# Performance work log

Hardware: AMD Instinct MI355X
Metric: run time of the kernel (lower is better)

The kernel has to match this reference:

```python
import jax, jax.numpy as jnp
import numpy as np
from jax import lax

B, CIN, COUT, H, W = 2, 256, 128, 128, 128
PPI = 4  # pixels_per_iter


def setup_inputs() -> dict:
    key = jax.random.key(0)
    ks = jax.random.split(key, 10)
    p = lambda k, shp: jax.random.normal(k, shp, jnp.float32) * 0.05
    return {
        "x": jax.random.normal(ks[0], (B, CIN, H, W), jnp.float32),
        "grads": jax.random.normal(ks[1], (B, 2, H, W), jnp.float32),
        "w1": p(ks[2], (COUT, CIN, 1, 1)),          # conv1x1 (bias=False, resnet-style)
        "w2": p(ks[3], (COUT, CIN, 1, 1)),
        "merge_dw": p(ks[4], (2 * COUT, 1, 3, 3)),   # depthwise 3x3
        "merge_pw": p(ks[5], (COUT, 2 * COUT, 1, 1)),# pointwise 1x1
        "merge_b": p(ks[6], (COUT,)),
        "post_dw": p(ks[7], (COUT, 1, 3, 3)),
        "post_pw": p(ks[8], (COUT, COUT, 1, 1)),
        "post_b": p(ks[9], (COUT,)),
    }


def conv2d(x, w, pad=0, groups=1):
    return lax.conv_general_dilated(x, w, (1, 1), [(pad, pad), (pad, pad)],
                                    feature_group_count=groups)


def base_grid(Bn, Hn, Wn):
    # torch affine_grid with identity theta, align_corners=True
    xs = jnp.linspace(-1.0, 1.0, Wn)
    ys = jnp.linspace(-1.0, 1.0, Hn)
    gx, gy = jnp.meshgrid(xs, ys)                      # [H,W] each
    g = jnp.stack([gx, gy], axis=-1)                   # [H,W,2], last dim = (x,y)
    return jnp.broadcast_to(g, (Bn, Hn, Wn, 2))


def grid_sample(img, grid):
    # bilinear, align_corners=True, padding_mode='zeros' (torch defaults)
    Bn, C, Hn, Wn = img.shape
    x = (grid[..., 0] + 1.0) * (Wn - 1) * 0.5          # [B,H,W] pixel coords
    y = (grid[..., 1] + 1.0) * (Hn - 1) * 0.5
    x0 = jnp.floor(x); y0 = jnp.floor(y)
    x1 = x0 + 1.0;     y1 = y0 + 1.0
    wx1 = x - x0; wx0 = 1.0 - wx1
    wy1 = y - y0; wy0 = 1.0 - wy1

    def corner(xi, yi, w):
        valid = (xi >= 0) & (xi <= Wn - 1) & (yi >= 0) & (yi <= Hn - 1)
        xc = jnp.clip(xi, 0, Wn - 1).astype(jnp.int32)
        yc = jnp.clip(yi, 0, Hn - 1).astype(jnp.int32)
        v = jax.vmap(lambda im, yy, xx: im[:, yy, xx])(img, yc, xc)  # [B,C,H,W]
        return v * (w * valid)[:, None]

    return (corner(x0, y0, wx0 * wy0) + corner(x1, y0, wx1 * wy0) +
            corner(x0, y1, wx0 * wy1) + corner(x1, y1, wx1 * wy1))


def reference(x, grads, w1, w2, merge_dw, merge_pw, merge_b, post_dw, post_pw, post_b):
    Bn, _, Hn, Wn = x.shape
    iters = 3 * Hn // (4 * PPI)
    g = (1.5 * grads / iters).transpose(0, 2, 3, 1)    # [B,H,W,2]
    grid = base_grid(Bn, Hn, Wn)
    grid1 = grid + g
    grid2 = grid - g

    m1 = jax.nn.sigmoid(conv2d(x, w1))
    m2 = jax.nn.sigmoid(conv2d(x, w2))

    def step(carry, _):
        a, b, sa, sb = carry
        a = grid_sample(a, grid1)
        b = grid_sample(b, grid2)
        return (a, b, sa + a, sb + b), None

    (_, _, s1, s2), _ = lax.scan(jax.checkpoint(step), (m1, m2, m1, m2), None, length=iters)

    m = jnp.concatenate([jax.nn.sigmoid(s1), jax.nn.sigmoid(s2)], axis=1)  # [B,2*COUT,H,W]
    m = conv2d(conv2d(m, merge_dw, pad=1, groups=2 * COUT), merge_pw) + merge_b[None, :, None, None]
    m = conv2d(conv2d(m, post_dw, pad=1, groups=COUT), post_pw) + post_b[None, :, None, None]
    return m
```

## Files before the change

### kernel.cpp

```cpp
#include <hip/hip_runtime.h>
#include <hip/hip_fp16.h>


#define PC 4194304
#define HW 16384

struct CoefC { int4 o0; float4 w0; int4 o1; float4 w1; int4 o2; float4 w2; int4 o3; float4 w3; };
struct Coef1 { int4 oa; float4 wa; };

struct alignas(16) H8 { __half2 h[4]; };
struct alignas(8)  H4 { __half2 h[2]; };
typedef _Float16 f16x8 __attribute__((ext_vector_type(8)));
typedef float f32x4 __attribute__((ext_vector_type(4)));

__device__ __forceinline__ float sigf(float v) { return 1.0f / (1.0f + __expf(-v)); }

__device__ __forceinline__ H8 f8h(const float* f) {
  H8 r;
#pragma unroll
  for (int i = 0; i < 4; i++) r.h[i] = __floats2half2_rn(f[2*i], f[2*i+1]);
  return r;
}
__device__ __forceinline__ f16x8 ld8(const __half* p) { return *(const f16x8*)p; }
__device__ __forceinline__ void fma8(float* a, const f16x8& v, float w) {
#pragma unroll
  for (int i = 0; i < 8; i++) a[i] = fmaf(w, (float)v[i], a[i]);
}
__device__ __forceinline__ void fma4g(float* a, const f16x8& v0, const f16x8& v1,
                                      const f16x8& v2, const f16x8& v3, float4 w) {
  fma8(a, v0, w.x); fma8(a, v1, w.y); fma8(a, v2, w.z); fma8(a, v3, w.w);
}

template <int SPB>
__device__ __forceinline__ int slot_base_64k(int bid) {
  int xcd = bid & 7;
  int i = xcd >> 1;
  int half = xcd & 1;
  int sub = bid >> 3;
  return (i >> 1) * 32768 + (i & 1) * 16384 + half * 8192 + sub * SPB;
}
template <int SPB>
__device__ __forceinline__ int slot_base_32k(int bid) {
  int xcd = bid & 7;
  int b = xcd >> 2;
  int q = xcd & 3;
  int sub = bid >> 3;
  return b * 16384 + q * 4096 + sub * SPB;
}

__device__ __forceinline__ void stencil(const float* __restrict__ g, float sgn, int pix,
                                        int4& op, float4& wt) {
  int b = pix >> 14, hw = pix & 16383;
  int h = hw >> 7, w = hw & 127;
  float gx = g[(size_t)(b * 2 + 0) * HW + hw];
  float gy = g[(size_t)(b * 2 + 1) * HW + hw];
  float xp = (float)w + sgn * gx;
  float yp = (float)h + sgn * gy;
  float x0f = floorf(xp), y0f = floorf(yp);
  float fx = xp - x0f, fy = yp - y0f;
  int x0 = (int)x0f, y0 = (int)y0f;
  int x1 = x0 + 1, y1 = y0 + 1;
  bool vx0 = (x0 >= 0) && (x0 <= 127);
  bool vx1 = (x1 >= 0) && (x1 <= 127);
  bool vy0 = (y0 >= 0) && (y0 <= 127);
  bool vy1 = (y1 >= 0) && (y1 <= 127);
  int x0c = min(max(x0, 0), 127), x1c = min(max(x1, 0), 127);
  int y0c = min(max(y0, 0), 127), y1c = min(max(y1, 0), 127);
  int bb = b << 14;
  op.x = bb + y0c * 128 + x0c;
  op.y = bb + y0c * 128 + x1c;
  op.z = bb + y1c * 128 + x0c;
  op.w = bb + y1c * 128 + x1c;
  wt.x = (vx0 && vy0) ? (1.f - fx) * (1.f - fy) : 0.f;
  wt.y = (vx1 && vy0) ? fx * (1.f - fy) : 0.f;
  wt.z = (vx0 && vy1) ? (1.f - fx) * fy : 0.f;
  wt.w = (vx1 && vy1) ? fx * fy : 0.f;
}

__device__ __forceinline__ int4 shl7(int4 v) {
  return make_int4(v.x << 7, v.y << 7, v.z << 7, v.w << 7);
}
__device__ __forceinline__ float4 scale4(float4 v, float s) {
  return make_float4(v.x * s, v.y * s, v.z * s, v.w * s);
}

__global__ __launch_bounds__(256) void prep_kernel(const float* __restrict__ grads,
                                                   Coef1* __restrict__ c1,
                                                   CoefC* __restrict__ c2,
                                                   const float* __restrict__ mdw,
                                                   const float* __restrict__ pdw,
                                                   const float* __restrict__ w1,
                                                   const float* __restrict__ w2,
                                                   const float* __restrict__ mpw,
                                                   const float* __restrict__ ppw,
                                                   float* __restrict__ wdwT,
                                                   float* __restrict__ pdwT,
                                                   __half* __restrict__ wT16,
                                                   __half* __restrict__ wpw1,
                                                   __half* __restrict__ wpw2) {
  int bid = blockIdx.x;
  int tid = threadIdx.x;
  if (bid < 256) {
    int idx = bid * 256 + tid;
    int chain = idx >> 15;
    int p = idx & 32767;
    float sgn = chain ? -3.96875f : 3.96875f;
    int4 op; float4 ow;
    stencil(grads, sgn, p, op, ow);
    Coef1 a; a.oa = shl7(op); a.wa = ow;
    c1[idx] = a;
    CoefC c;
    int4 o2; float4 nw;
    stencil(grads, sgn, op.x, o2, nw); c.o0 = shl7(o2); c.w0 = scale4(nw, ow.x);
    stencil(grads, sgn, op.y, o2, nw); c.o1 = shl7(o2); c.w1 = scale4(nw, ow.y);
    stencil(grads, sgn, op.z, o2, nw); c.o2 = shl7(o2); c.w2 = scale4(nw, ow.z);
    stencil(grads, sgn, op.w, o2, nw); c.o3 = shl7(o2); c.w3 = scale4(nw, ow.w);
    c2[idx] = c;
  } else {
    int i = (bid - 256) * 256 + tid;
    if (i < 65536) {
      int co = i >> 8, ci = i & 255;
      float v = (co < 128) ? w1[co * 256 + ci] : w2[(size_t)(co - 128) * 256 + ci];
      wT16[i] = __float2half(v);
    } else if (i < 98304) {
      int j = i - 65536;
      wpw1[j] = __float2half(mpw[j]);
    } else if (i < 114688) {
      int j = i - 98304;
      wpw2[j] = __float2half(ppw[j]);
    } else if (i < 116992) {
      int j = i - 114688;
      int ch = j / 9, t = j % 9;
      wdwT[t * 256 + ch] = mdw[j];
    } else if (i < 118144) {
      int j = i - 116992;
      int ch = j / 9, t = j % 9;
      pdwT[t * 128 + ch] = pdw[j];
    }
  }
}

__global__ __launch_bounds__(256) void conv1_kernel(const float* __restrict__ x,
                                                    const __half* __restrict__ wT16,
                                                    __half* __restrict__ mOut) {
  __shared__ __align__(16) char As[4096];
  __shared__ __align__(16) char Bs[16384];
  int tid = threadIdx.x;
  int p0 = blockIdx.x * 64;
  int b = p0 >> 14;
  int hw0 = p0 & 16383;
  int wv = tid >> 6, ln = tid & 63;
  int hi = ln >> 4, lo = ln & 15;
  f32x4 acc[4][4] = {};
  const float* xb = x + (size_t)b * 256 * HW + hw0;
  int apx = tid & 63, ac8 = (tid >> 6) * 8;
  int abyte = (apx * 64 + ac8 * 2) ^ ((apx & 3) << 4);
  for (int k = 0; k < 256; k += 32) {
    f16x8 av;
#pragma unroll
    for (int j = 0; j < 8; j++) av[j] = (_Float16)xb[(size_t)(k + ac8 + j) * HW + apx];
    if (k) __syncthreads();
    *(f16x8*)(As + abyte) = av;
    {
      const __half* src = wT16 + (size_t)tid * 256 + k;
#pragma unroll
      for (int s = 0; s < 4; s++) {
        f16x8 bv = *(const f16x8*)(src + s * 8);
        int byte = (tid * 64 + s * 16) ^ ((tid & 3) << 4);
        *(f16x8*)(Bs + byte) = bv;
      }
    }
    __syncthreads();
    f16x8 aF[4], bF[4];
#pragma unroll
    for (int m = 0; m < 4; m++) {
      int px = m * 16 + lo;
      int byte = (px * 64 + hi * 16) ^ ((px & 3) << 4);
      aF[m] = *(const f16x8*)(As + byte);
    }
#pragma unroll
    for (int n = 0; n < 4; n++) {
      int co = wv * 64 + n * 16 + lo;
      int byte = (co * 64 + hi * 16) ^ ((co & 3) << 4);
      bF[n] = *(const f16x8*)(Bs + byte);
    }
#pragma unroll
    for (int m = 0; m < 4; m++)
#pragma unroll
      for (int n = 0; n < 4; n++)
        acc[m][n] = __builtin_amdgcn_mfma_f32_16x16x32_f16(aF[m], bF[n], acc[m][n], 0, 0, 0);
  }
  size_t base = (wv >= 2) ? (size_t)PC : 0;
  int col0 = (wv & 1) * 64;
#pragma unroll
  for (int m = 0; m < 4; m++)
#pragma unroll
    for (int n = 0; n < 4; n++) {
      int col = col0 + n * 16 + lo;
#pragma unroll
      for (int rr = 0; rr < 4; rr++) {
        int px = p0 + m * 16 + hi * 4 + rr;
        mOut[base + (size_t)px * 128 + col] = __float2half(sigf(acc[m][n][rr]));
      }
    }
}

template <int ACC>
__global__ __launch_bounds__(256) void s2_kernel(const __half* __restrict__ inb,
                                                 __half* __restrict__ outb,
                                                 const __half* __restrict__ accAdd,
                                                 __half* __restrict__ accOut,
                                                 const uint4* __restrict__ c2tab) {
  __shared__ uint4 cs[128];
  int tid = threadIdx.x;
  int slot0 = slot_base_64k<16>(blockIdx.x);
  if (tid < 128) cs[tid] = c2tab[(size_t)slot0 * 8 + tid];
  __syncthreads();
  const CoefC c = ((const CoefC*)cs)[tid >> 4];
  int slot = slot0 + (tid >> 4);
  int ch = (tid & 15) << 3;
  int chain = slot >> 15;
  size_t cb = (size_t)chain * PC;
  const __half* base = inb + cb + ch;
  int rowel = ((slot & 32767) << 7) + ch;

  float a2[8] = {};
  f16x8 p0 = ld8(base + c.o0.x), p1 = ld8(base + c.o0.y),
        p2 = ld8(base + c.o0.z), p3 = ld8(base + c.o0.w);
  f16x8 q0 = ld8(base + c.o1.x), q1 = ld8(base + c.o1.y),
        q2 = ld8(base + c.o1.z), q3 = ld8(base + c.o1.w);
  fma4g(a2, p0, p1, p2, p3, c.w0);
  p0 = ld8(base + c.o2.x); p1 = ld8(base + c.o2.y);
  p2 = ld8(base + c.o2.z); p3 = ld8(base + c.o2.w);
  fma4g(a2, q0, q1, q2, q3, c.w1);
  q0 = ld8(base + c.o3.x); q1 = ld8(base + c.o3.y);
  q2 = ld8(base + c.o3.z); q3 = ld8(base + c.o3.w);
  fma4g(a2, p0, p1, p2, p3, c.w2);
  fma4g(a2, q0, q1, q2, q3, c.w3);

  if (ACC != 3) *(H8*)(outb + cb + rowel) = f8h(a2);
  if (ACC == 1 || ACC == 3) {
    f16x8 av = ld8(accAdd + cb + rowel);
    float af[8];
#pragma unroll
    for (int i = 0; i < 8; i++) af[i] = a2[i] + (float)av[i];
    *(H8*)(accOut + cb + rowel) = f8h(af);
  } else if (ACC == 2) {
    f16x8 av = ld8(accOut + cb + rowel);
    float af[8];
#pragma unroll
    for (int i = 0; i < 8; i++) af[i] = a2[i] + (float)av[i];
    *(H8*)(accOut + cb + rowel) = f8h(af);
  }
}

template <int MODE>
__global__ __launch_bounds__(256) void s1_kernel(const __half* __restrict__ tin,
                                                 const __half* __restrict__ own,
                                                 __half* __restrict__ outb,
                                                 const uint4* __restrict__ c1tab) {
  __shared__ uint4 cs[32];
  int tid = threadIdx.x;
  int slot0 = slot_base_64k<16>(blockIdx.x);
  if (tid < 32) cs[tid] = c1tab[(size_t)slot0 * 2 + tid];
  __syncthreads();
  const Coef1 a = ((const Coef1*)cs)[tid >> 4];
  int slot = slot0 + (tid >> 4);
  int ch = (tid & 15) << 3;
  int chain = slot >> 15;
  size_t cb = (size_t)chain * PC;
  const __half* base = tin + cb + ch;
  int rowel = ((slot & 32767) << 7) + ch;
  f16x8 t0 = ld8(base + a.oa.x), t1 = ld8(base + a.oa.y),
        t2 = ld8(base + a.oa.z), t3 = ld8(base + a.oa.w);
  f16x8 ov = ld8(own + cb + rowel);
  float r[8] = {};
  fma4g(r, t0, t1, t2, t3, a.wa);
  if (MODE == 0) {
#pragma unroll
    for (int i = 0; i < 8; i++) r[i] += (float)ov[i];
  } else {
#pragma unroll
    for (int i = 0; i < 8; i++) r[i] = sigf(r[i] + (float)ov[i]);
  }
  *(H8*)(outb + cb + rowel) = f8h(r);
}

template <int C>
__global__ __launch_bounds__(256) void dw_kernel(const __half* __restrict__ in,
                                                 const float* __restrict__ wT,
                                                 __half* __restrict__ out) {
  int tid = threadIdx.x;
  constexpr int TPP = C / 8;
  constexpr int PPB = 256 / TPP;
  int slot = slot_base_32k<PPB>(blockIdx.x) + tid / TPP;
  int ch = (tid % TPP) * 8;
  int b = slot >> 14, h = (slot >> 7) & 127, w = slot & 127;
  const __half* src;
  int choff;
  if (C == 256) { src = in + ((ch < 128) ? 0 : (size_t)PC); choff = ch & 127; }
  else          { src = in; choff = ch; }
  float acc[8] = {};
#pragma unroll
  for (int t = 0; t < 9; t++) {
    int dy = t / 3 - 1, dx = t % 3 - 1;
    int yy = h + dy, xx = w + dx;
    if (yy < 0 || yy > 127 || xx < 0 || xx > 127) continue;
    int q = (b << 14) + yy * 128 + xx;
    f16x8 v = ld8(src + (size_t)q * 128 + choff);
    float4 wa = *(const float4*)(wT + t * C + ch);
    float4 wb = *(const float4*)(wT + t * C + ch + 4);
    acc[0] = fmaf(wa.x, (float)v[0], acc[0]);
    acc[1] = fmaf(wa.y, (float)v[1], acc[1]);
    acc[2] = fmaf(wa.z, (float)v[2], acc[2]);
    acc[3] = fmaf(wa.w, (float)v[3], acc[3]);
    acc[4] = fmaf(wb.x, (float)v[4], acc[4]);
    acc[5] = fmaf(wb.y, (float)v[5], acc[5]);
    acc[6] = fmaf(wb.z, (float)v[6], acc[6]);
    acc[7] = fmaf(wb.w, (float)v[7], acc[7]);
  }
  *(H8*)(out + (size_t)slot * C + ch) = f8h(acc);
}

__global__ __launch_bounds__(256) void pw1_kernel(const __half* __restrict__ in,
                                                  const __half* __restrict__ w16,
                                                  const float* __restrict__ bias,
                                                  __half* __restrict__ out) {
  int tid = threadIdx.x;
  int p0 = blockIdx.x * 64;
  int wv = tid >> 6, ln = tid & 63;
  int hi = ln >> 4, lo = ln & 15;
  int px = p0 + wv * 16 + lo;
  f32x4 acc[8] = {};
  for (int k = 0; k < 256; k += 32) {
    f16x8 bF = *(const f16x8*)(in + (size_t)px * 256 + k + hi * 8);
#pragma unroll
    for (int m = 0; m < 8; m++) {
      f16x8 aF = *(const f16x8*)(w16 + (size_t)(m * 16 + lo) * 256 + k + hi * 8);
      acc[m] = __builtin_amdgcn_mfma_f32_16x16x32_f16(aF, bF, acc[m], 0, 0, 0);
    }
  }
  int opx = p0 + wv * 16 + lo;
#pragma unroll
  for (int m = 0; m < 8; m++) {
    int co = m * 16 + hi * 4;
    float4 bv = *(const float4*)(bias + co);
    H4 hv;
    hv.h[0] = __floats2half2_rn(acc[m][0] + bv.x, acc[m][1] + bv.y);
    hv.h[1] = __floats2half2_rn(acc[m][2] + bv.z, acc[m][3] + bv.w);
    *(H4*)(out + (size_t)opx * 128 + co) = hv;
  }
}

__global__ __launch_bounds__(256) void pw2_kernel(const __half* __restrict__ in,
                                                  const __half* __restrict__ w16,
                                                  const float* __restrict__ bias,
                                                  float* __restrict__ out) {
  int tid = threadIdx.x;
  int p0 = blockIdx.x * 64;
  int b = p0 >> 14;
  int hw0 = p0 & 16383;
  int wv = tid >> 6, ln = tid & 63;
  int hi = ln >> 4, lo = ln & 15;
  int co0 = wv * 32;
  f32x4 acc[4][2] = {};
  for (int k = 0; k < 128; k += 32) {
    f16x8 aF[4], bF[2];
#pragma unroll
    for (int m = 0; m < 4; m++)
      aF[m] = *(const f16x8*)(in + (size_t)(p0 + m * 16 + lo) * 128 + k + hi * 8);
#pragma unroll
    for (int n = 0; n < 2; n++)
      bF[n] = *(const f16x8*)(w16 + (size_t)(co0 + n * 16 + lo) * 128 + k + hi * 8);
#pragma unroll
    for (int m = 0; m < 4; m++)
#pragma unroll
      for (int n = 0; n < 2; n++)
        acc[m][n] = __builtin_amdgcn_mfma_f32_16x16x32_f16(aF[m], bF[n], acc[m][n], 0, 0, 0);
  }
#pragma unroll
  for (int m = 0; m < 4; m++)
#pragma unroll
    for (int n = 0; n < 2; n++) {
      int co = co0 + n * 16 + lo;
      float bb = bias[co];
      float4 v = {acc[m][n][0] + bb, acc[m][n][1] + bb, acc[m][n][2] + bb, acc[m][n][3] + bb};
      *(float4*)(out + (size_t)(b * 128 + co) * HW + hw0 + m * 16 + hi * 4) = v;
    }
}

extern "C" void kernel_launch(void* const* d_in, const int* in_sizes, int n_in,
                              void* d_out, int out_size, void* d_ws, size_t ws_size,
                              hipStream_t stream) {
  const float* x     = (const float*)d_in[0];
  const float* grads = (const float*)d_in[1];
  const float* w1    = (const float*)d_in[2];
  const float* w2    = (const float*)d_in[3];
  const float* mdw   = (const float*)d_in[4];
  const float* mpw   = (const float*)d_in[5];
  const float* mb    = (const float*)d_in[6];
  const float* pdw   = (const float*)d_in[7];
  const float* ppw   = (const float*)d_in[8];
  const float* pb    = (const float*)d_in[9];
  float* out = (float*)d_out;
  char* wsb = (char*)d_ws;

  __half* M  = (__half*)wsb;
  __half* A  = (__half*)(wsb + (size_t)16777216);
  __half* Bb = (__half*)(wsb + (size_t)33554432);
  __half* Pb = (__half*)(wsb + (size_t)50331648);
  __half* Qb = (__half*)(wsb + (size_t)67108864);
  CoefC* C2  = (CoefC*)(wsb + (size_t)83886080);
  Coef1* C1  = (Coef1*)(wsb + (size_t)92274688);
  __half* WT16 = (__half*)(wsb + (size_t)94371840);
  __half* WPW1 = (__half*)(wsb + (size_t)94502912);
  __half* WPW2 = (__half*)(wsb + (size_t)94568448);
  float* wdwT  = (float*)(wsb + (size_t)94601216);
  float* pdwT  = wdwT + 2304;

  const uint4* c2u = (const uint4*)C2;
  const uint4* c1u = (const uint4*)C1;

  prep_kernel<<<718, 256, 0, stream>>>(grads, C1, C2, mdw, pdw, w1, w2, mpw, ppw,
                                       wdwT, pdwT, WT16, WPW1, WPW2);
  conv1_kernel<<<512, 256, 0, stream>>>(x, WT16, M);

  s2_kernel<0><<<4096, 256, 0, stream>>>(M,  A,  nullptr, nullptr, c2u);
  s2_kernel<0><<<4096, 256, 0, stream>>>(A,  Bb, nullptr, nullptr, c2u);
  s2_kernel<0><<<4096, 256, 0, stream>>>(Bb, A,  nullptr, nullptr, c2u);
  s2_kernel<1><<<4096, 256, 0, stream>>>(A,  Bb, M,       Pb,      c2u);
  s2_kernel<0><<<4096, 256, 0, stream>>>(Bb, A,  nullptr, nullptr, c2u);
  s2_kernel<0><<<4096, 256, 0, stream>>>(A,  Bb, nullptr, nullptr, c2u);
  s2_kernel<0><<<4096, 256, 0, stream>>>(Bb, A,  nullptr, nullptr, c2u);
  s2_kernel<2><<<4096, 256, 0, stream>>>(A,  Bb, nullptr, Pb,      c2u);
  s2_kernel<0><<<4096, 256, 0, stream>>>(Pb, A,  nullptr, nullptr, c2u);
  s2_kernel<1><<<4096, 256, 0, stream>>>(A,  Bb, Pb,      Qb,      c2u);
  s2_kernel<3><<<4096, 256, 0, stream>>>(Qb, A,  Qb,      Pb,      c2u);
  s1_kernel<0><<<4096, 256, 0, stream>>>(Pb, Pb, Bb, c1u);
  s1_kernel<1><<<4096, 256, 0, stream>>>(Bb, M,  A,  c1u);

  __half* DW1 = Bb;
  __half* PW1 = Qb;
  __half* DW2 = Qb + PC;
  dw_kernel<256><<<4096, 256, 0, stream>>>(A, wdwT, DW1);
  pw1_kernel<<<512, 256, 0, stream>>>(DW1, WPW1, mb, PW1);
  dw_kernel<128><<<2048, 256, 0, stream>>>(PW1, pdwT, DW2);
  pw2_kernel<<<512, 256, 0, stream>>>(DW2, WPW2, pb, out);
}
```

Baseline: 269.0 us.

## Fuse depthwise 3x3 convs into pointwise MFMA kernels via swizzled LDS tiles

Merges each depthwise 3x3 conv with the following pointwise 1x1 MFMA GEMM into a single kernel. Each block computes an 8x8 pixel tile's depthwise outputs for all channels into XOR-swizzled shared memory, then runs the MFMA GEMM from LDS. This removes the global write and read of the DW1/DW2 intermediates and two kernel launches. In exchange there are fewer blocks (512 instead of 4096/2048), a serial per-thread channel loop, and 32KB/16KB of LDS per block, which may lower occupancy and latency hiding.

```diff
diff --git a/kernel.cpp b/kernel.cpp
--- a/kernel.cpp
+++ b/kernel.cpp
@@ -38,14 +38,6 @@
   int half = xcd & 1;
   int sub = bid >> 3;
   return (i >> 1) * 32768 + (i & 1) * 16384 + half * 8192 + sub * SPB;
-}
-template <int SPB>
-__device__ __forceinline__ int slot_base_32k(int bid) {
-  int xcd = bid & 7;
-  int b = xcd >> 2;
-  int q = xcd & 3;
-  int sub = bid >> 3;
-  return b * 16384 + q * 4096 + sub * SPB;
 }
 
 __device__ __forceinline__ void stencil(const float* __restrict__ g, float sgn, int pix,
@@ -286,89 +278,129 @@
   *(H8*)(outb + cb + rowel) = f8h(r);
 }
 
-template <int C>
-__global__ __launch_bounds__(256) void dw_kernel(const __half* __restrict__ in,
-                                                 const float* __restrict__ wT,
-                                                 __half* __restrict__ out) {
-  int tid = threadIdx.x;
-  constexpr int TPP = C / 8;
-  constexpr int PPB = 256 / TPP;
-  int slot = slot_base_32k<PPB>(blockIdx.x) + tid / TPP;
-  int ch = (tid % TPP) * 8;
-  int b = slot >> 14, h = (slot >> 7) & 127, w = slot & 127;
-  const __half* src;
-  int choff;
-  if (C == 256) { src = in + ((ch < 128) ? 0 : (size_t)PC); choff = ch & 127; }
-  else          { src = in; choff = ch; }
-  float acc[8] = {};
-#pragma unroll
-  for (int t = 0; t < 9; t++) {
-    int dy = t / 3 - 1, dx = t % 3 - 1;
-    int yy = h + dy, xx = w + dx;
-    if (yy < 0 || yy > 127 || xx < 0 || xx > 127) continue;
-    int q = (b << 14) + yy * 128 + xx;
-    f16x8 v = ld8(src + (size_t)q * 128 + choff);
-    float4 wa = *(const float4*)(wT + t * C + ch);
-    float4 wb = *(const float4*)(wT + t * C + ch + 4);
-    acc[0] = fmaf(wa.x, (float)v[0], acc[0]);
-    acc[1] = fmaf(wa.y, (float)v[1], acc[1]);
-    acc[2] = fmaf(wa.z, (float)v[2], acc[2]);
-    acc[3] = fmaf(wa.w, (float)v[3], acc[3]);
-    acc[4] = fmaf(wb.x, (float)v[4], acc[4]);
-    acc[5] = fmaf(wb.y, (float)v[5], acc[5]);
-    acc[6] = fmaf(wb.z, (float)v[6], acc[6]);
-    acc[7] = fmaf(wb.w, (float)v[7], acc[7]);
-  }
-  *(H8*)(out + (size_t)slot * C + ch) = f8h(acc);
-}
-
-__global__ __launch_bounds__(256) void pw1_kernel(const __half* __restrict__ in,
-                                                  const __half* __restrict__ w16,
-                                                  const float* __restrict__ bias,
-                                                  __half* __restrict__ out) {
-  int tid = threadIdx.x;
-  int p0 = blockIdx.x * 64;
+__global__ __launch_bounds__(256) void merge1_kernel(const __half* __restrict__ A,
+                                                     const float* __restrict__ wT,
+                                                     const __half* __restrict__ w16,
+                                                     const float* __restrict__ bias,
+                                                     __half* __restrict__ PW1) {
+  __shared__ __align__(16) char lds[32768];
+  int tid = threadIdx.x;
+  int bid = blockIdx.x;
+  int xcd = bid & 7;
+  int b = xcd >> 2, q = xcd & 3;
+  int sub = bid >> 3;
+  int orow = q * 32 + (sub >> 4) * 8;
+  int ocol = (sub & 15) * 8;
+  int pxl = tid & 63;
+  int r = pxl >> 3, cc = pxl & 7;
+  int h = orow + r, w = ocol + cc;
+  int ch0 = (tid >> 6) * 64;
+  for (int cg = 0; cg < 8; cg++) {
+    int ch = ch0 + cg * 8;
+    const __half* src = A + ((ch < 128) ? 0 : (size_t)PC);
+    int choff = ch & 127;
+    float acc[8] = {};
+#pragma unroll
+    for (int t = 0; t < 9; t++) {
+      int dy = t / 3 - 1, dx = t % 3 - 1;
+      int yy = h + dy, xx = w + dx;
+      if (yy < 0 || yy > 127 || xx < 0 || xx > 127) continue;
+      int qp = (b << 14) + yy * 128 + xx;
+      f16x8 v = ld8(src + (size_t)qp * 128 + choff);
+      float4 wa = *(const float4*)(wT + t * 256 + ch);
+      float4 wb = *(const float4*)(wT + t * 256 + ch + 4);
+      acc[0] = fmaf(wa.x, (float)v[0], acc[0]);
+      acc[1] = fmaf(wa.y, (float)v[1], acc[1]);
+      acc[2] = fmaf(wa.z, (float)v[2], acc[2]);
+      acc[3] = fmaf(wa.w, (float)v[3], acc[3]);
+      acc[4] = fmaf(wb.x, (float)v[4], acc[4]);
+      acc[5] = fmaf(wb.y, (float)v[5], acc[5]);
+      acc[6] = fmaf(wb.z, (float)v[6], acc[6]);
+      acc[7] = fmaf(wb.w, (float)v[7], acc[7]);
+    }
+    int byte = (pxl * 512 + ch * 2) ^ ((pxl & 7) << 4);
+    *(H8*)(lds + byte) = f8h(acc);
+  }
+  __syncthreads();
   int wv = tid >> 6, ln = tid & 63;
   int hi = ln >> 4, lo = ln & 15;
-  int px = p0 + wv * 16 + lo;
-  f32x4 acc[8] = {};
+  int pxw = wv * 16 + lo;
+  f32x4 acc2[8] = {};
   for (int k = 0; k < 256; k += 32) {
-    f16x8 bF = *(const f16x8*)(in + (size_t)px * 256 + k + hi * 8);
+    int byte = (pxw * 512 + (k + hi * 8) * 2) ^ ((pxw & 7) << 4);
+    f16x8 bF = *(const f16x8*)(lds + byte);
 #pragma unroll
     for (int m = 0; m < 8; m++) {
       f16x8 aF = *(const f16x8*)(w16 + (size_t)(m * 16 + lo) * 256 + k + hi * 8);
-      acc[m] = __builtin_amdgcn_mfma_f32_16x16x32_f16(aF, bF, acc[m], 0, 0, 0);
-    }
-  }
-  int opx = p0 + wv * 16 + lo;
+      acc2[m] = __builtin_amdgcn_mfma_f32_16x16x32_f16(aF, bF, acc2[m], 0, 0, 0);
+    }
+  }
+  int opx = (b << 14) + (orow + (pxw >> 3)) * 128 + ocol + (pxw & 7);
 #pragma unroll
   for (int m = 0; m < 8; m++) {
     int co = m * 16 + hi * 4;
     float4 bv = *(const float4*)(bias + co);
     H4 hv;
-    hv.h[0] = __floats2half2_rn(acc[m][0] + bv.x, acc[m][1] + bv.y);
-    hv.h[1] = __floats2half2_rn(acc[m][2] + bv.z, acc[m][3] + bv.w);
-    *(H4*)(out + (size_t)opx * 128 + co) = hv;
-  }
-}
-
-__global__ __launch_bounds__(256) void pw2_kernel(const __half* __restrict__ in,
-                                                  const __half* __restrict__ w16,
-                                                  const float* __restrict__ bias,
-                                                  float* __restrict__ out) {
-  int tid = threadIdx.x;
-  int p0 = blockIdx.x * 64;
-  int b = p0 >> 14;
-  int hw0 = p0 & 16383;
+    hv.h[0] = __floats2half2_rn(acc2[m][0] + bv.x, acc2[m][1] + bv.y);
+    hv.h[1] = __floats2half2_rn(acc2[m][2] + bv.z, acc2[m][3] + bv.w);
+    *(H4*)(PW1 + (size_t)opx * 128 + co) = hv;
+  }
+}
+
+__global__ __launch_bounds__(256) void merge2_kernel(const __half* __restrict__ PW1,
+                                                     const float* __restrict__ wT,
+                                                     const __half* __restrict__ w16,
+                                                     const float* __restrict__ bias,
+                                                     float* __restrict__ out) {
+  __shared__ __align__(16) char lds[16384];
+  int tid = threadIdx.x;
+  int bid = blockIdx.x;
+  int xcd = bid & 7;
+  int b = xcd >> 2, q = xcd & 3;
+  int sub = bid >> 3;
+  int orow = q * 32 + (sub >> 4) * 8;
+  int ocol = (sub & 15) * 8;
+  int pxl = tid & 63;
+  int r = pxl >> 3, cc = pxl & 7;
+  int h = orow + r, w = ocol + cc;
+  int ch0 = (tid >> 6) * 32;
+  for (int cg = 0; cg < 4; cg++) {
+    int ch = ch0 + cg * 8;
+    float acc[8] = {};
+#pragma unroll
+    for (int t = 0; t < 9; t++) {
+      int dy = t / 3 - 1, dx = t % 3 - 1;
+      int yy = h + dy, xx = w + dx;
+      if (yy < 0 || yy > 127 || xx < 0 || xx > 127) continue;
+      int qp = (b << 14) + yy * 128 + xx;
+      f16x8 v = ld8(PW1 + (size_t)qp * 128 + ch);
+      float4 wa = *(const float4*)(wT + t * 128 + ch);
+      float4 wb = *(const float4*)(wT + t * 128 + ch + 4);
+      acc[0] = fmaf(wa.x, (float)v[0], acc[0]);
+      acc[1] = fmaf(wa.y, (float)v[1], acc[1]);
+      acc[2] = fmaf(wa.z, (float)v[2], acc[2]);
+      acc[3] = fmaf(wa.w, (float)v[3], acc[3]);
+      acc[4] = fmaf(wb.x, (float)v[4], acc[4]);
+      acc[5] = fmaf(wb.y, (float)v[5], acc[5]);
+      acc[6] = fmaf(wb.z, (float)v[6], acc[6]);
+      acc[7] = fmaf(wb.w, (float)v[7], acc[7]);
+    }
+    int byte = (pxl * 256 + ch * 2) ^ ((pxl & 7) << 4);
+    *(H8*)(lds + byte) = f8h(acc);
+  }
+  __syncthreads();
   int wv = tid >> 6, ln = tid & 63;
   int hi = ln >> 4, lo = ln & 15;
   int co0 = wv * 32;
-  f32x4 acc[4][2] = {};
+  f32x4 acc2[4][2] = {};
   for (int k = 0; k < 128; k += 32) {
     f16x8 aF[4], bF[2];
 #pragma unroll
-    for (int m = 0; m < 4; m++)
-      aF[m] = *(const f16x8*)(in + (size_t)(p0 + m * 16 + lo) * 128 + k + hi * 8);
+    for (int m = 0; m < 4; m++) {
+      int px = m * 16 + lo;
+      int byte = (px * 256 + (k + hi * 8) * 2) ^ ((px & 7) << 4);
+      aF[m] = *(const f16x8*)(lds + byte);
+    }
 #pragma unroll
     for (int n = 0; n < 2; n++)
       bF[n] = *(const f16x8*)(w16 + (size_t)(co0 + n * 16 + lo) * 128 + k + hi * 8);
@@ -376,7 +408,7 @@
     for (int m = 0; m < 4; m++)
 #pragma unroll
       for (int n = 0; n < 2; n++)
-        acc[m][n] = __builtin_amdgcn_mfma_f32_16x16x32_f16(aF[m], bF[n], acc[m][n], 0, 0, 0);
+        acc2[m][n] = __builtin_amdgcn_mfma_f32_16x16x32_f16(aF[m], bF[n], acc2[m][n], 0, 0, 0);
   }
 #pragma unroll
   for (int m = 0; m < 4; m++)
@@ -384,8 +416,10 @@
     for (int n = 0; n < 2; n++) {
       int co = co0 + n * 16 + lo;
       float bb = bias[co];
-      float4 v = {acc[m][n][0] + bb, acc[m][n][1] + bb, acc[m][n][2] + bb, acc[m][n][3] + bb};
-      *(float4*)(out + (size_t)(b * 128 + co) * HW + hw0 + m * 16 + hi * 4) = v;
+      float4 v = {acc2[m][n][0] + bb, acc2[m][n][1] + bb,
+                  acc2[m][n][2] + bb, acc2[m][n][3] + bb};
+      int hw = (orow + 2 * m + (hi >> 1)) * 128 + ocol + (hi & 1) * 4;
+      *(float4*)(out + (size_t)(b * 128 + co) * HW + hw) = v;
     }
 }
 
@@ -439,11 +473,6 @@
   s1_kernel<0><<<4096, 256, 0, stream>>>(Pb, Pb, Bb, c1u);
   s1_kernel<1><<<4096, 256, 0, stream>>>(Bb, M,  A,  c1u);
 
-  __half* DW1 = Bb;
-  __half* PW1 = Qb;
-  __half* DW2 = Qb + PC;
-  dw_kernel<256><<<4096, 256, 0, stream>>>(A, wdwT, DW1);
-  pw1_kernel<<<512, 256, 0, stream>>>(DW1, WPW1, mb, PW1);
-  dw_kernel<128><<<2048, 256, 0, stream>>>(PW1, pdwT, DW2);
-  pw2_kernel<<<512, 256, 0, stream>>>(DW2, WPW2, pb, out);
-}
+  merge1_kernel<<<512, 256, 0, stream>>>(A, wdwT, WPW1, mb, Qb);
+  merge2_kernel<<<512, 256, 0, stream>>>(Qb, pdwT, WPW2, pb, out);
+}
```

After: 290.2 us. +7.9%, slower.

## Split s2 gather taps across half-warps and reduce with shuffle

Applied to the files above, without the earlier changes.

Restructures the two-step bilinear gather kernel so that each 32-lane group handles two slots, and each half of the group gathers 8 of that slot's 16 taps. Partial sums are combined with a cross-lane shuffle, and only the lower half writes results. This is meant to raise memory-level parallelism per thread and add occupancy hints through launch_bounds(256,4). In exchange it adds shuffle work, idles half the lanes during stores, and uses more registers per thread.

```diff
diff --git a/kernel.cpp b/kernel.cpp
--- a/kernel.cpp
+++ b/kernel.cpp
@@ -206,51 +206,85 @@
 }
 
 template <int ACC>
-__global__ __launch_bounds__(256) void s2_kernel(const __half* __restrict__ inb,
-                                                 __half* __restrict__ outb,
-                                                 const __half* __restrict__ accAdd,
-                                                 __half* __restrict__ accOut,
-                                                 const uint4* __restrict__ c2tab) {
+__global__ __launch_bounds__(256, 4) void s2_kernel(const __half* __restrict__ inb,
+                                                    __half* __restrict__ outb,
+                                                    const __half* __restrict__ accAdd,
+                                                    __half* __restrict__ accOut,
+                                                    const uint4* __restrict__ c2tab) {
   __shared__ uint4 cs[128];
   int tid = threadIdx.x;
   int slot0 = slot_base_64k<16>(blockIdx.x);
   if (tid < 128) cs[tid] = c2tab[(size_t)slot0 * 8 + tid];
   __syncthreads();
-  const CoefC c = ((const CoefC*)cs)[tid >> 4];
-  int slot = slot0 + (tid >> 4);
-  int ch = (tid & 15) << 3;
-  int chain = slot >> 15;
+  int sg = tid >> 5;
+  int lane = tid & 31;
+  int side = lane >> 4;
+  int ch = (lane & 15) << 3;
+  const CoefC cA = ((const CoefC*)cs)[sg];
+  const CoefC cB = ((const CoefC*)cs)[sg + 8];
+  int slotA = slot0 + sg;
+  int slotB = slot0 + sg + 8;
+  int chain = slot0 >> 15;
   size_t cb = (size_t)chain * PC;
   const __half* base = inb + cb + ch;
-  int rowel = ((slot & 32767) << 7) + ch;
-
-  float a2[8] = {};
-  f16x8 p0 = ld8(base + c.o0.x), p1 = ld8(base + c.o0.y),
-        p2 = ld8(base + c.o0.z), p3 = ld8(base + c.o0.w);
-  f16x8 q0 = ld8(base + c.o1.x), q1 = ld8(base + c.o1.y),
-        q2 = ld8(base + c.o1.z), q3 = ld8(base + c.o1.w);
-  fma4g(a2, p0, p1, p2, p3, c.w0);
-  p0 = ld8(base + c.o2.x); p1 = ld8(base + c.o2.y);
-  p2 = ld8(base + c.o2.z); p3 = ld8(base + c.o2.w);
-  fma4g(a2, q0, q1, q2, q3, c.w1);
-  q0 = ld8(base + c.o3.x); q1 = ld8(base + c.o3.y);
-  q2 = ld8(base + c.o3.z); q3 = ld8(base + c.o3.w);
-  fma4g(a2, p0, p1, p2, p3, c.w2);
-  fma4g(a2, q0, q1, q2, q3, c.w3);
-
-  if (ACC != 3) *(H8*)(outb + cb + rowel) = f8h(a2);
-  if (ACC == 1 || ACC == 3) {
-    f16x8 av = ld8(accAdd + cb + rowel);
-    float af[8];
-#pragma unroll
-    for (int i = 0; i < 8; i++) af[i] = a2[i] + (float)av[i];
-    *(H8*)(accOut + cb + rowel) = f8h(af);
-  } else if (ACC == 2) {
-    f16x8 av = ld8(accOut + cb + rowel);
-    float af[8];
-#pragma unroll
-    for (int i = 0; i < 8; i++) af[i] = a2[i] + (float)av[i];
-    *(H8*)(accOut + cb + rowel) = f8h(af);
+  int rowA = ((slotA & 32767) << 7) + ch;
+  int rowB = ((slotB & 32767) << 7) + ch;
+
+  int aO0 = side ? cA.o0.y : cA.o0.x;  float aW0 = side ? cA.w0.y : cA.w0.x;
+  int aO1 = side ? cA.o0.w : cA.o0.z;  float aW1 = side ? cA.w0.w : cA.w0.z;
+  int aO2 = side ? cA.o1.y : cA.o1.x;  float aW2 = side ? cA.w1.y : cA.w1.x;
+  int aO3 = side ? cA.o1.w : cA.o1.z;  float aW3 = side ? cA.w1.w : cA.w1.z;
+  int aO4 = side ? cA.o2.y : cA.o2.x;  float aW4 = side ? cA.w2.y : cA.w2.x;
+  int aO5 = side ? cA.o2.w : cA.o2.z;  float aW5 = side ? cA.w2.w : cA.w2.z;
+  int aO6 = side ? cA.o3.y : cA.o3.x;  float aW6 = side ? cA.w3.y : cA.w3.x;
+  int aO7 = side ? cA.o3.w : cA.o3.z;  float aW7 = side ? cA.w3.w : cA.w3.z;
+  int bO0 = side ? cB.o0.y : cB.o0.x;  float bW0 = side ? cB.w0.y : cB.w0.x;
+  int bO1 = side ? cB.o0.w : cB.o0.z;  float bW1 = side ? cB.w0.w : cB.w0.z;
+  int bO2 = side ? cB.o1.y : cB.o1.x;  float bW2 = side ? cB.w1.y : cB.w1.x;
+  int bO3 = side ? cB.o1.w : cB.o1.z;  float bW3 = side ? cB.w1.w : cB.w1.z;
+  int bO4 = side ? cB.o2.y : cB.o2.x;  float bW4 = side ? cB.w2.y : cB.w2.x;
+  int bO5 = side ? cB.o2.w : cB.o2.z;  float bW5 = side ? cB.w2.w : cB.w2.z;
+  int bO6 = side ? cB.o3.y : cB.o3.x;  float bW6 = side ? cB.w3.y : cB.w3.x;
+  int bO7 = side ? cB.o3.w : cB.o3.z;  float bW7 = side ? cB.w3.w : cB.w3.z;
+
+  f16x8 a0 = ld8(base + aO0), a1 = ld8(base + aO1), a2v = ld8(base + aO2), a3 = ld8(base + aO3);
+  f16x8 a4 = ld8(base + aO4), a5 = ld8(base + aO5), a6 = ld8(base + aO6), a7 = ld8(base + aO7);
+  f16x8 b0 = ld8(base + bO0), b1 = ld8(base + bO1), b2 = ld8(base + bO2), b3 = ld8(base + bO3);
+  f16x8 b4 = ld8(base + bO4), b5 = ld8(base + bO5), b6 = ld8(base + bO6), b7 = ld8(base + bO7);
+
+  float sA[8] = {}, sB[8] = {};
+  fma8(sA, a0, aW0); fma8(sA, a1, aW1); fma8(sA, a2v, aW2); fma8(sA, a3, aW3);
+  fma8(sA, a4, aW4); fma8(sA, a5, aW5); fma8(sA, a6, aW6); fma8(sA, a7, aW7);
+  fma8(sB, b0, bW0); fma8(sB, b1, bW1); fma8(sB, b2, bW2); fma8(sB, b3, bW3);
+  fma8(sB, b4, bW4); fma8(sB, b5, bW5); fma8(sB, b6, bW6); fma8(sB, b7, bW7);
+#pragma unroll
+  for (int i = 0; i < 8; i++) {
+    sA[i] += __shfl_xor(sA[i], 16);
+    sB[i] += __shfl_xor(sB[i], 16);
+  }
+
+  if (side == 0) {
+    if (ACC != 3) {
+      *(H8*)(outb + cb + rowA) = f8h(sA);
+      *(H8*)(outb + cb + rowB) = f8h(sB);
+    }
+    if (ACC == 1 || ACC == 3) {
+      f16x8 vA = ld8(accAdd + cb + rowA);
+      f16x8 vB = ld8(accAdd + cb + rowB);
+      float fA[8], fB[8];
+#pragma unroll
+      for (int i = 0; i < 8; i++) { fA[i] = sA[i] + (float)vA[i]; fB[i] = sB[i] + (float)vB[i]; }
+      *(H8*)(accOut + cb + rowA) = f8h(fA);
+      *(H8*)(accOut + cb + rowB) = f8h(fB);
+    } else if (ACC == 2) {
+      f16x8 vA = ld8(accOut + cb + rowA);
+      f16x8 vB = ld8(accOut + cb + rowB);
+      float fA[8], fB[8];
+#pragma unroll
+      for (int i = 0; i < 8; i++) { fA[i] = sA[i] + (float)vA[i]; fB[i] = sB[i] + (float)vB[i]; }
+      *(H8*)(accOut + cb + rowA) = f8h(fA);
+      *(H8*)(accOut + cb + rowB) = f8h(fB);
+    }
   }
 }
 
```

Result: no change. 270.4 us (+0.5%).
